# Optimization experiments

Hardware: AMD Instinct MI355X
Metric: run time of the kernel (lower is better)

The kernel has to match this reference:

```python
import jax, jax.numpy as jnp
import numpy as np


def setup_inputs() -> dict:
    key = jax.random.key(0)
    k1, k2 = jax.random.split(key)
    WS, M, K, N = 8, 8192, 512, 1024  # world_size, tokens, local-K, N
    inp = jax.random.normal(k1, (WS, M, K), dtype=jnp.float32)
    weight = jax.random.normal(k2, (WS, N, K), dtype=jnp.float32) * 0.02
    return {"input": inp, "weight": weight}


def reference(input, weight):
    # Per-rank partial GEMM: input [ws, M, K] x weight [ws, N, K] -> [ws, M, N]
    ws, M, _ = input.shape
    N = weight.shape[1]
    Ms = M // ws  # rows per rank after reduce-scatter
    partial = jnp.einsum("wmk,wnk->wmn", input, weight)
    # Reduce-scatter over M dim: rank r receives sum over ranks of rows [r*Ms:(r+1)*Ms]
    # partial -> [src_rank=ws, dst_rank=ws, Ms, N], sum over src_rank
    out = partial.reshape(ws, ws, Ms, N).sum(axis=0)  # [ws, Ms, N]
    return out
```

## Files before the change

### kernel.cpp

```cpp
#include <hip/hip_runtime.h>
#include <hip/hip_bf16.h>


#define WS 8
#define MM 8192
#define KK 512
#define NN 1024
#define KTOT (WS * KK)
#define BM 128
#define BN 64
#define BK 64

#define A_ELEMS ((size_t)WS * MM * KK)
#define B_ELEMS ((size_t)WS * NN * KK)
#define WS_NEEDED ((A_ELEMS + B_ELEMS) * 2)

typedef __attribute__((ext_vector_type(8))) short short8;
typedef __attribute__((ext_vector_type(4))) short short4v;
typedef __attribute__((ext_vector_type(4))) float floatx4;

static __device__ inline short f2bf(float f) {
    union { __hip_bfloat16 h; short s; } u;
    u.h = __float2bfloat16(f);
    return u.s;
}

static __device__ inline void glds16(const short* g, short* l) {
    __builtin_amdgcn_global_load_lds(
        (const __attribute__((address_space(1))) unsigned int*)(uintptr_t)g,
        (__attribute__((address_space(3))) unsigned int*)(uintptr_t)l,
        16, 0, 0);
}

#define CVT_ABLOCKS 16384
#define CVT_NBLOCKS 18432

__global__ __launch_bounds__(256)
void cvt_f32_bf16(const float* __restrict__ A, const float* __restrict__ B,
                  short* __restrict__ Abf, short* __restrict__ Bbf) {
    const float* src;
    short* dst;
    size_t base;
    if (blockIdx.x < CVT_ABLOCKS) {
        src = A; dst = Abf;
        base = ((size_t)blockIdx.x * 256 + threadIdx.x) * 8;
    } else {
        src = B; dst = Bbf;
        base = ((size_t)(blockIdx.x - CVT_ABLOCKS) * 256 + threadIdx.x) * 8;
    }
    float4 v0 = *(const float4*)(src + base);
    float4 v1 = *(const float4*)(src + base + 4);
    short8 o = { f2bf(v0.x), f2bf(v0.y), f2bf(v0.z), f2bf(v0.w),
                 f2bf(v1.x), f2bf(v1.y), f2bf(v1.z), f2bf(v1.w) };
    *(short8*)(dst + base) = o;
}

__global__ __launch_bounds__(256, 4)
void gemm_bf16_rs(const short* __restrict__ Abf, const short* __restrict__ Bbf,
                  float* __restrict__ C) {
    __shared__ short As[BM * BK];
    __shared__ short Bs[BN * BK];

    const int tid  = threadIdx.x;
    const int lane = tid & 63;
    const int wid  = tid >> 6;
    const int m0 = blockIdx.y * BM;
    const int n0 = blockIdx.x * BN;
    const int wr = wid >> 1, wc = wid & 1;
    const int lm = lane & 15, quad = lane >> 4;

    const int lrow = lane >> 3;
    const int ss   = (lane & 7) ^ lrow;

    size_t gA[4], gB[2];
#pragma unroll
    for (int t = 0; t < 4; ++t)
        gA[t] = (size_t)(m0 + wid * 32 + t * 8 + lrow) * KK + ss * 8;
#pragma unroll
    for (int t = 0; t < 2; ++t)
        gB[t] = (size_t)(n0 + wid * 16 + t * 8 + lrow) * KK + ss * 8;

    floatx4 acc[4][2];
#pragma unroll
    for (int i = 0; i < 4; ++i)
#pragma unroll
        for (int j = 0; j < 2; ++j) acc[i][j] = (floatx4)0.f;

    for (int kt = 0; kt < KTOT; kt += BK) {
        const int w  = kt >> 9;
        const int kk = kt & (KK - 1);
        const short* Aw = Abf + (size_t)w * MM * KK + kk;
        const short* Bw = Bbf + (size_t)w * NN * KK + kk;

        __syncthreads();
#pragma unroll
        for (int t = 0; t < 4; ++t)
            glds16(Aw + gA[t], &As[(wid * 4 + t) * 512 + lane * 8]);
#pragma unroll
        for (int t = 0; t < 2; ++t)
            glds16(Bw + gB[t], &Bs[(wid * 2 + t) * 512 + lane * 8]);
        __syncthreads();

        short8 af[2][4], bfr[2][2];
#pragma unroll
        for (int kc = 0; kc < 2; ++kc) {
#pragma unroll
            for (int i = 0; i < 4; ++i) {
                const int row = wr * 64 + i * 16 + lm;
                const int sa  = (kc * 4 + quad) ^ (lm & 7);
                af[kc][i] = *(const short8*)&As[row * BK + sa * 8];
            }
#pragma unroll
            for (int j = 0; j < 2; ++j) {
                const int row = wc * 32 + j * 16 + lm;
                const int sb  = (kc * 4 + quad) ^ (lm & 7);
                bfr[kc][j] = *(const short8*)&Bs[row * BK + sb * 8];
            }
        }
#pragma unroll
        for (int kc = 0; kc < 2; ++kc)
#pragma unroll
            for (int i = 0; i < 4; ++i)
#pragma unroll
                for (int j = 0; j < 2; ++j)
                    acc[i][j] = __builtin_amdgcn_mfma_f32_16x16x32_bf16(
                        af[kc][i], bfr[kc][j], acc[i][j], 0, 0, 0);
    }

#pragma unroll
    for (int i = 0; i < 4; ++i)
#pragma unroll
        for (int j = 0; j < 2; ++j) {
            const int n = n0 + wc * 32 + j * 16 + lm;
#pragma unroll
            for (int r = 0; r < 4; ++r) {
                const int m = m0 + wr * 64 + i * 16 + quad * 4 + r;
                C[(size_t)m * NN + n] = acc[i][j][r];
            }
        }
}

__global__ __launch_bounds__(256, 2)
void gemm_rs_fused(const float* __restrict__ A, const float* __restrict__ B,
                   float* __restrict__ C) {
    __shared__ short As[128 * 32];
    __shared__ short Bs[128 * 32];
    const int tid = threadIdx.x;
    const int m0 = blockIdx.y * 128;
    const int n0 = blockIdx.x * 128;
    const int wid = tid >> 6, lane = tid & 63;
    const int wr = wid >> 1, wc = wid & 1;
    const int lm = lane & 15, quad = lane >> 4;
    floatx4 acc[4][4];
#pragma unroll
    for (int i = 0; i < 4; ++i)
#pragma unroll
        for (int j = 0; j < 4; ++j) acc[i][j] = (floatx4)0.f;
    for (int kt = 0; kt < KTOT; kt += 32) {
        const int w = kt >> 9, kk = kt & (KK - 1);
        const float* Aw = A + (size_t)w * MM * KK;
        const float* Bw = B + (size_t)w * NN * KK;
        __syncthreads();
#pragma unroll
        for (int i = 0; i < 4; ++i) {
            const int idx = i * 256 + tid;
            const int row = idx >> 3;
            const int c4 = (idx & 7) * 4;
            float4 av = *(const float4*)&Aw[(size_t)(m0 + row) * KK + kk + c4];
            float4 bv = *(const float4*)&Bw[(size_t)(n0 + row) * KK + kk + c4];
            short4v a4 = { f2bf(av.x), f2bf(av.y), f2bf(av.z), f2bf(av.w) };
            short4v b4 = { f2bf(bv.x), f2bf(bv.y), f2bf(bv.z), f2bf(bv.w) };
            *(short4v*)&As[row * 32 + c4] = a4;
            *(short4v*)&Bs[row * 32 + c4] = b4;
        }
        __syncthreads();
        short8 af[4], bfr[4];
#pragma unroll
        for (int i = 0; i < 4; ++i)
            af[i] = *(const short8*)&As[(wr * 64 + i * 16 + lm) * 32 + quad * 8];
#pragma unroll
        for (int j = 0; j < 4; ++j)
            bfr[j] = *(const short8*)&Bs[(wc * 64 + j * 16 + lm) * 32 + quad * 8];
#pragma unroll
        for (int i = 0; i < 4; ++i)
#pragma unroll
            for (int j = 0; j < 4; ++j)
                acc[i][j] = __builtin_amdgcn_mfma_f32_16x16x32_bf16(
                    af[i], bfr[j], acc[i][j], 0, 0, 0);
    }
#pragma unroll
    for (int i = 0; i < 4; ++i)
#pragma unroll
        for (int j = 0; j < 4; ++j) {
            const int n = n0 + wc * 64 + j * 16 + lm;
#pragma unroll
            for (int r = 0; r < 4; ++r) {
                const int m = m0 + wr * 64 + i * 16 + quad * 4 + r;
                C[(size_t)m * NN + n] = acc[i][j][r];
            }
        }
}

extern "C" void kernel_launch(void* const* d_in, const int* in_sizes, int n_in,
                              void* d_out, int out_size, void* d_ws, size_t ws_size,
                              hipStream_t stream) {
    const float* A = (const float*)d_in[0];
    const float* B = (const float*)d_in[1];
    float* C = (float*)d_out;

    if (ws_size >= WS_NEEDED) {
        short* Abf = (short*)d_ws;
        short* Bbf = Abf + A_ELEMS;
        cvt_f32_bf16<<<CVT_NBLOCKS, 256, 0, stream>>>(A, B, Abf, Bbf);
        dim3 grid(NN / BN, MM / BM);
        gemm_bf16_rs<<<grid, 256, 0, stream>>>(Abf, Bbf, C);
    } else {
        dim3 grid(NN / 128, MM / 128);
        gemm_rs_fused<<<grid, 256, 0, stream>>>(A, B, C);
    }
}
```

Measured before the change: 299.9 us.

## Double-buffer LDS tiles in bf16 GEMM to overlap global loads with MFMA

Adds a two-stage LDS ping-pong buffer to the bf16 GEMM. The next K-tile's global-to-LDS loads are issued before computing the current tile, with manual vmcnt waits and barriers in place of __syncthreads, to hide memory latency. Doubling LDS use lowers the occupancy hint from 4 to 3 blocks per CU. On the last iteration the loop wraps and issues a redundant prefetch of tile 0. The hand-written waitcnt and barrier asm is fragile if the compiler schedules memory operations differently than assumed.

Result: no change. 301.8 us (+0.6%).

```diff
diff --git a/kernel.cpp b/kernel.cpp
--- a/kernel.cpp
+++ b/kernel.cpp
@@ -10,6 +10,7 @@
 #define BM 128
 #define BN 64
 #define BK 64
+#define ITERS (KTOT / BK)
 
 #define A_ELEMS ((size_t)WS * MM * KK)
 #define B_ELEMS ((size_t)WS * NN * KK)
@@ -55,11 +56,11 @@
     *(short8*)(dst + base) = o;
 }
 
-__global__ __launch_bounds__(256, 4)
+__global__ __launch_bounds__(256, 3)
 void gemm_bf16_rs(const short* __restrict__ Abf, const short* __restrict__ Bbf,
                   float* __restrict__ C) {
-    __shared__ short As[BM * BK];
-    __shared__ short Bs[BN * BK];
+    __shared__ short As[2][BM * BK];
+    __shared__ short Bs[2][BN * BK];
 
     const int tid  = threadIdx.x;
     const int lane = tid & 63;
@@ -86,20 +87,31 @@
 #pragma unroll
         for (int j = 0; j < 2; ++j) acc[i][j] = (floatx4)0.f;
 
-    for (int kt = 0; kt < KTOT; kt += BK) {
-        const int w  = kt >> 9;
-        const int kk = kt & (KK - 1);
-        const short* Aw = Abf + (size_t)w * MM * KK + kk;
-        const short* Bw = Bbf + (size_t)w * NN * KK + kk;
-
-        __syncthreads();
-#pragma unroll
-        for (int t = 0; t < 4; ++t)
-            glds16(Aw + gA[t], &As[(wid * 4 + t) * 512 + lane * 8]);
-#pragma unroll
-        for (int t = 0; t < 2; ++t)
-            glds16(Bw + gB[t], &Bs[(wid * 2 + t) * 512 + lane * 8]);
-        __syncthreads();
+#pragma unroll
+    for (int q = 0; q < 4; ++q)
+        glds16(Abf + gA[q], &As[0][(wid * 4 + q) * 512 + lane * 8]);
+#pragma unroll
+    for (int q = 0; q < 2; ++q)
+        glds16(Bbf + gB[q], &Bs[0][(wid * 2 + q) * 512 + lane * 8]);
+
+    for (int t = 0; t < ITERS; ++t) {
+        const int p  = t & 1;
+        const int tn = (t + 1) & (ITERS - 1);
+        const int np = tn & 1;
+        const int wn = tn >> 3;
+        const int kn = (tn & 7) * BK;
+        const short* Aw = Abf + (size_t)wn * MM * KK + kn;
+        const short* Bw = Bbf + (size_t)wn * NN * KK + kn;
+
+#pragma unroll
+        for (int q = 0; q < 4; ++q)
+            glds16(Aw + gA[q], &As[np][(wid * 4 + q) * 512 + lane * 8]);
+#pragma unroll
+        for (int q = 0; q < 2; ++q)
+            glds16(Bw + gB[q], &Bs[np][(wid * 2 + q) * 512 + lane * 8]);
+
+        asm volatile("s_waitcnt vmcnt(6)" ::: "memory");
+        asm volatile("s_barrier" ::: "memory");
 
         short8 af[2][4], bfr[2][2];
 #pragma unroll
@@ -108,13 +120,13 @@
             for (int i = 0; i < 4; ++i) {
                 const int row = wr * 64 + i * 16 + lm;
                 const int sa  = (kc * 4 + quad) ^ (lm & 7);
-                af[kc][i] = *(const short8*)&As[row * BK + sa * 8];
+                af[kc][i] = *(const short8*)&As[p][row * BK + sa * 8];
             }
 #pragma unroll
             for (int j = 0; j < 2; ++j) {
                 const int row = wc * 32 + j * 16 + lm;
                 const int sb  = (kc * 4 + quad) ^ (lm & 7);
-                bfr[kc][j] = *(const short8*)&Bs[row * BK + sb * 8];
+                bfr[kc][j] = *(const short8*)&Bs[p][row * BK + sb * 8];
             }
         }
 #pragma unroll
@@ -125,6 +137,8 @@
                 for (int j = 0; j < 2; ++j)
                     acc[i][j] = __builtin_amdgcn_mfma_f32_16x16x32_bf16(
                         af[kc][i], bfr[kc][j], acc[i][j], 0, 0, 0);
+
+        asm volatile("s_barrier" ::: "memory");
     }
 
 #pragma unroll
```
